# Performance work log

Hardware: AMD Instinct MI355X
Metric: run time of the kernel (lower is better)

Reference implementation:

```python
import jax, jax.numpy as jnp
import numpy as np

TAU = 0.5

def setup_inputs() -> dict:
    key = jax.random.key(0)
    ks = jax.random.split(key, 20)
    B, D1, D2, E1, E2, U = 4096, 2000, 2000, 256, 256, 512
    M = E1 + E2
    s = lambda k, shp, scale=0.05: jax.random.normal(k, shp, dtype=jnp.float32) * scale
    return {
        "inputs": jax.random.normal(ks[0], (B, D1 + D2), dtype=jnp.float32),
        "h_tm1": jax.random.normal(ks[1], (B, U), dtype=jnp.float32),
        "crohis_tm": jax.random.normal(ks[2], (B, M), dtype=jnp.float32),
        "embed_weight_1": s(ks[3], (D1, E1)),
        "embed_weight_2": s(ks[4], (D2, E2)),
        "ca_1to2_w": s(ks[5], (E1, E1)),
        "ca_1to2_u": s(ks[6], (E2, E1)),
        "ca_1to2_v": s(ks[7], (E2, E1)),
        "ca_2to1_w": s(ks[8], (E2, E2)),
        "ca_2to1_u": s(ks[9], (E1, E2)),
        "ca_2to1_v": s(ks[10], (E1, E2)),
        "crohis_weight_w": s(ks[11], (M, U)),
        "crohis_bias": jnp.zeros((U,), jnp.float32),
        "crohis_decomp_weight": s(ks[12], (M, M)),
        "crohis_decomp_bias": jnp.zeros((M,), jnp.float32),
        "kernel": s(ks[13], (M, 3 * U)),
        "recurrent_kernel": s(ks[14], (U, 3 * U)),
        "bias": jnp.zeros((3 * U,), jnp.float32),
    }


def reference(inputs, h_tm1, crohis_tm,
              embed_weight_1, embed_weight_2,
              ca_1to2_w, ca_1to2_u, ca_1to2_v,
              ca_2to1_w, ca_2to1_u, ca_2to1_v,
              crohis_weight_w, crohis_bias,
              crohis_decomp_weight, crohis_decomp_bias,
              kernel, recurrent_kernel, bias):
    D1 = embed_weight_1.shape[0]
    U = recurrent_kernel.shape[0]
    # dual embedding lookups (dense multi-hot x embedding matrix)
    seqx1 = inputs[:, :D1]
    seqx2 = inputs[:, D1:]
    emb1 = seqx1 @ embed_weight_1   # [B, E1]
    emb2 = seqx2 @ embed_weight_2   # [B, E2]
    # cross-attention gates (softmax over feature axis, as K.softmax default)
    att12 = jax.nn.softmax(jnp.tanh(emb1 @ ca_1to2_w + emb2 @ ca_1to2_u) * (emb2 @ ca_1to2_v), axis=-1)
    att21 = jax.nn.softmax(jnp.tanh(emb2 @ ca_2to1_w + emb1 @ ca_2to1_u) * (emb1 @ ca_2to1_v), axis=-1)
    x = jnp.concatenate([emb1 * att12, emb2 * att21], axis=-1)  # [B, M]
    # cross-history decomposition modulating previous hidden state
    cro = jnp.tanh(crohis_tm @ crohis_decomp_weight + crohis_decomp_bias)
    h_prev = h_tm1 + jnp.tanh(cro @ crohis_weight_w + crohis_bias)
    # GRU (implementation=2, reset_after=False)
    mx = x @ kernel + bias                         # [B, 3U]
    x_z, x_r, x_h = mx[:, :U], mx[:, U:2 * U], mx[:, 2 * U:]
    mi = h_prev @ recurrent_kernel[:, :2 * U]      # [B, 2U]
    z = jax.nn.sigmoid(x_z + mi[:, :U])
    r = jax.nn.sigmoid(x_r + mi[:, U:])
    hh = jnp.tanh(x_h + (r * h_prev) @ recurrent_kernel[:, 2 * U:])
    h = z * h_prev + (1.0 - z) * hh
    # updated cross-history state (exponential moving average with tau)
    crohis_new = TAU * crohis_tm + (1.0 - TAU) * x
    return h, crohis_new
```

## Files before the change

### kernel.cpp

```cpp
#include <hip/hip_runtime.h>
#include <hip/hip_bf16.h>
#include <math.h>


#define TAU_F 0.5f

typedef __bf16 bf16x8 __attribute__((ext_vector_type(8)));
typedef __bf16 bf16x4 __attribute__((ext_vector_type(4)));
typedef float f32x4 __attribute__((ext_vector_type(4)));

__device__ __forceinline__ void gload16(const void* g, void* l) {
    __builtin_amdgcn_global_load_lds(
        (const __attribute__((address_space(1))) void*)g,
        (__attribute__((address_space(3))) void*)l, 16, 0, 0);
}

struct SubGemm {
    const void* A;
    int lda;
    int Kvalid;
    const __bf16* BT;
    int ldbt;
    float* C;
    int ldc;
    long long strideC;
    int Ksub;
    int nbx;
    int pairSplit;
    int pairAOff;
};

template <bool AFP32>
__global__ __launch_bounds__(256) void gemm_dual(SubGemm g1, SubGemm g2, int blocks1)
{
    __shared__ __bf16 As[3][64][32];
    __shared__ __bf16 Bs[3][128][32];

    const int tid = threadIdx.x, w = tid >> 6, l = tid & 63;

    const int gx = gridDim.x;
    const int nwg = gx * (int)gridDim.y;
    const int hw = (int)blockIdx.y * gx + (int)blockIdx.x;
    const int lg = (hw & 7) * (nwg >> 3) + (hw >> 3);
    const int bxl_lin = lg % gx;
    const int by = lg / gx;

    const bool second = bxl_lin >= blocks1;
    const SubGemm& g = second ? g2 : g1;
    const int bxl = second ? bxl_lin - blocks1 : bxl_lin;
    const int ct = bxl % g.nbx, spl = bxl / g.nbx;
    const int brow = by * 64, bcol = ct * 128;
    const int k_begin = spl * g.Ksub;
    const int nt = g.Ksub >> 5;
    float* C = g.C + (size_t)spl * g.strideC;
    const int aoff = (ct >= g.pairSplit) ? g.pairAOff : 0;

    const int sar = w * 16 + (l >> 2);
    const int sbr = w * 32 + (l >> 2);
    const int seg = (l & 3) * 8;

    const float*  AfRow = (const float*)g.A + aoff + (size_t)(brow + sar) * g.lda;
    const __bf16* AbRow = (const __bf16*)g.A + aoff + (size_t)(brow + sar) * g.lda + seg + k_begin;
    const __bf16* Bg0 = g.BT + (size_t)(bcol + sbr) * g.ldbt + seg + k_begin;
    const __bf16* Bg1 = Bg0 + (size_t)16 * g.ldbt;
    const int kcl = g.Kvalid - 8;

    f32x4 acc[2][4] = {};
    const int fr = l & 15, fk = (l >> 4) * 8;
    const int wr = (w >> 1) * 32, wc = (w & 1) * 64;

    f32x4 v0, v1;
    if constexpr (AFP32) {
        { int col = k_begin + seg; col = col < kcl ? col : kcl;
          v0 = *(const f32x4*)(AfRow + col); v1 = *(const f32x4*)(AfRow + col + 4); }
        gload16(Bg0, &Bs[0][w * 32][0]);
        gload16(Bg1, &Bs[0][w * 32 + 16][0]);
        asm volatile("s_waitcnt vmcnt(2)" ::: "memory");
        { __bf16 o[8];
#pragma unroll
          for (int z = 0; z < 4; ++z) { o[z] = (__bf16)v0[z]; o[4 + z] = (__bf16)v1[z]; }
          *(bf16x8*)&As[0][sar][seg] = *(bf16x8*)o; }
        { int col = k_begin + 32 + seg; col = col < kcl ? col : kcl;
          v0 = *(const f32x4*)(AfRow + col); v1 = *(const f32x4*)(AfRow + col + 4); }
        gload16(Bg0 + 32, &Bs[1][w * 32][0]);
        gload16(Bg1 + 32, &Bs[1][w * 32 + 16][0]);
    } else {
        gload16(AbRow,      &As[0][w * 16][0]);
        gload16(Bg0,        &Bs[0][w * 32][0]);
        gload16(Bg1,        &Bs[0][w * 32 + 16][0]);
        gload16(AbRow + 32, &As[1][w * 16][0]);
        gload16(Bg0 + 32,   &Bs[1][w * 32][0]);
        gload16(Bg1 + 32,   &Bs[1][w * 32 + 16][0]);
    }

    int b0 = 0, b1 = 1, b2 = 2;
    for (int t = 0; t < nt; ++t) {
        if (t < nt - 1) {
            if constexpr (AFP32) asm volatile("s_waitcnt vmcnt(2)" ::: "memory");
            else                 asm volatile("s_waitcnt vmcnt(3)" ::: "memory");
        } else {
            asm volatile("s_waitcnt vmcnt(0)" ::: "memory");
        }
        asm volatile("s_waitcnt lgkmcnt(0)" ::: "memory");
        __builtin_amdgcn_s_barrier();

        bf16x8 a[2], b[4];
#pragma unroll
        for (int m = 0; m < 2; ++m) a[m] = *(const bf16x8*)&As[b0][wr + m * 16 + fr][fk];
#pragma unroll
        for (int n = 0; n < 4; ++n) b[n] = *(const bf16x8*)&Bs[b0][wc + n * 16 + fr][fk];

        if constexpr (AFP32) {
            if (t + 1 < nt) {
                __bf16 o[8];
#pragma unroll
                for (int z = 0; z < 4; ++z) { o[z] = (__bf16)v0[z]; o[4 + z] = (__bf16)v1[z]; }
                *(bf16x8*)&As[b1][sar][seg] = *(bf16x8*)o;
            }
            if (t + 2 < nt) {
                const int k = (t + 2) * 32;
                int col = k_begin + k + seg; col = col < kcl ? col : kcl;
                v0 = *(const f32x4*)(AfRow + col);
                v1 = *(const f32x4*)(AfRow + col + 4);
                gload16(Bg0 + k, &Bs[b2][w * 32][0]);
                gload16(Bg1 + k, &Bs[b2][w * 32 + 16][0]);
            }
        } else {
            if (t + 2 < nt) {
                const int k = (t + 2) * 32;
                gload16(AbRow + k, &As[b2][w * 16][0]);
                gload16(Bg0 + k,   &Bs[b2][w * 32][0]);
                gload16(Bg1 + k,   &Bs[b2][w * 32 + 16][0]);
            }
        }

#pragma unroll
        for (int m = 0; m < 2; ++m)
#pragma unroll
            for (int n = 0; n < 4; ++n)
                acc[m][n] = __builtin_amdgcn_mfma_f32_16x16x32_bf16(a[m], b[n], acc[m][n], 0, 0, 0);

        const int tmp = b0; b0 = b1; b1 = b2; b2 = tmp;
    }

    const int fq = (l >> 4) * 4;
#pragma unroll
    for (int m = 0; m < 2; ++m)
#pragma unroll
        for (int n = 0; n < 4; ++n)
#pragma unroll
            for (int r = 0; r < 4; ++r) {
                int row = brow + wr + m * 16 + fq + r;
                int col = bcol + wc + n * 16 + fr;
                C[(size_t)row * g.ldc + col] = acc[m][n][r];
            }
}

__global__ __launch_bounds__(256) void prep_w(
    const float* __restrict__ ew1, const float* __restrict__ ew2,
    const float* __restrict__ w12, const float* __restrict__ u12,
    const float* __restrict__ v12, const float* __restrict__ w21,
    const float* __restrict__ u21, const float* __restrict__ v21,
    const float* __restrict__ cd_w, const float* __restrict__ cw_w,
    const float* __restrict__ kern, const float* __restrict__ rkern,
    __bf16* __restrict__ WT, __bf16* __restrict__ WcatT,
    __bf16* __restrict__ cdT, __bf16* __restrict__ cwT,
    __bf16* __restrict__ kernT, __bf16* __restrict__ rkernT)
{
    int idx = blockIdx.x * 256 + threadIdx.x;
    if (idx < 1048576) {
        int n = idx >> 11, k = idx & 2047;
        float v = 0.f;
        if (k < 2000) v = (n < 256) ? ew1[(size_t)k * 256 + n]
                                    : ew2[(size_t)k * 256 + (n - 256)];
        WT[idx] = (__bf16)v;
        return;
    }
    idx -= 1048576;
    if (idx < 524288) {
        int n = idx >> 9, k = idx & 511;
        int jm = n & 255; bool khi = k >= 256; int kk = k & 255;
        float v;
        if (n < 256)      v = khi ? u12[kk * 256 + jm] : w12[kk * 256 + jm];
        else if (n < 512) v = khi ? w21[kk * 256 + jm] : u21[kk * 256 + jm];
        else if (n < 768) v = khi ? v12[kk * 256 + jm] : 0.f;
        else              v = khi ? 0.f : v21[kk * 256 + jm];
        WcatT[idx] = (__bf16)v;
        return;
    }
    idx -= 524288;
    if (idx < 262144) {
        int n = idx >> 9, k = idx & 511;
        cdT[idx] = (__bf16)cd_w[(size_t)k * 512 + n];
        return;
    }
    idx -= 262144;
    if (idx < 262144) {
        int n = idx >> 9, k = idx & 511;
        cwT[idx] = (__bf16)cw_w[(size_t)k * 512 + n];
        return;
    }
    idx -= 262144;
    if (idx < 786432) {
        int n = idx >> 9, k = idx & 511;
        kernT[idx] = (__bf16)kern[(size_t)k * 1536 + n];
        return;
    }
    idx -= 786432;
    if (idx < 786432) {
        int n = idx >> 9, k = idx & 511;
        rkernT[idx] = (__bf16)rkern[(size_t)k * 1536 + n];
    }
}

__global__ __launch_bounds__(256) void reduce_A(
    const float* __restrict__ P12, const float* __restrict__ P4,
    const float* __restrict__ cd_b,
    __bf16* __restrict__ E, __bf16* __restrict__ cro)
{
    int b = blockIdx.x;
    int i = (((b & 2047) * 256) + threadIdx.x) * 4;
    if (b < 2048) {
        f32x4 p0 = *(const f32x4*)(P12 + i);
        f32x4 p1 = *(const f32x4*)(P12 + (1 << 21) + i);
        __bf16 o[4];
#pragma unroll
        for (int j = 0; j < 4; ++j) o[j] = (__bf16)(p0[j] + p1[j]);
        *(bf16x4*)&E[i] = *(bf16x4*)o;
    } else {
        f32x4 p0 = *(const f32x4*)(P4 + i);
        int c = i & 511;
        __bf16 o[4];
#pragma unroll
        for (int j = 0; j < 4; ++j) o[j] = (__bf16)tanhf(p0[j] + cd_b[c + j]);
        *(bf16x4*)&cro[i] = *(bf16x4*)o;
    }
}

__global__ __launch_bounds__(256) void fuse1(
    const float* __restrict__ T, const __bf16* __restrict__ E,
    const float* __restrict__ crohis,
    const float* __restrict__ P5,
    const float* __restrict__ h_tm1, const float* __restrict__ cw_b,
    __bf16* __restrict__ x, float* __restrict__ cro_out,
    float* __restrict__ hprev, __bf16* __restrict__ hprev_bf)
{
    __shared__ float s4[4];
    int b = blockIdx.x;
    int j = threadIdx.x;
    if (b < 4096) {
        const float* t = T + (size_t)b * 1024;
        float s12 = tanhf(t[j])       * t[512 + j];
        float s21 = tanhf(t[256 + j]) * t[768 + j];
        float v = s12;
#pragma unroll
        for (int o = 32; o >= 1; o >>= 1) v = fmaxf(v, __shfl_xor(v, o, 64));
        __syncthreads(); if ((j & 63) == 0) s4[j >> 6] = v; __syncthreads();
        float m12 = fmaxf(fmaxf(s4[0], s4[1]), fmaxf(s4[2], s4[3]));
        float e12 = expf(s12 - m12);
        v = e12;
#pragma unroll
        for (int o = 32; o >= 1; o >>= 1) v += __shfl_xor(v, o, 64);
        __syncthreads(); if ((j & 63) == 0) s4[j >> 6] = v; __syncthreads();
        float sum12 = s4[0] + s4[1] + s4[2] + s4[3];
        v = s21;
#pragma unroll
        for (int o = 32; o >= 1; o >>= 1) v = fmaxf(v, __shfl_xor(v, o, 64));
        __syncthreads(); if ((j & 63) == 0) s4[j >> 6] = v; __syncthreads();
        float m21 = fmaxf(fmaxf(s4[0], s4[1]), fmaxf(s4[2], s4[3]));
        float e21 = expf(s21 - m21);
        v = e21;
#pragma unroll
        for (int o = 32; o >= 1; o >>= 1) v += __shfl_xor(v, o, 64);
        __syncthreads(); if ((j & 63) == 0) s4[j >> 6] = v; __syncthreads();
        float sum21 = s4[0] + s4[1] + s4[2] + s4[3];

        size_t b0 = (size_t)b * 512 + j, b1 = b0 + 256;
        float x1 = (float)E[b0] * (e12 / sum12);
        float x2 = (float)E[b1] * (e21 / sum21);
        x[b0] = (__bf16)x1;
        x[b1] = (__bf16)x2;
        cro_out[b0] = TAU_F * crohis[b0] + (1.f - TAU_F) * x1;
        cro_out[b1] = TAU_F * crohis[b1] + (1.f - TAU_F) * x2;
    } else {
        int i = ((b - 4096) * 256 + j) * 4;
        f32x4 p = *(const f32x4*)(P5 + i);
        f32x4 ht = *(const f32x4*)(h_tm1 + i);
        int c = i & 511;
        f32x4 o; __bf16 ob[4];
#pragma unroll
        for (int q = 0; q < 4; ++q) {
            float hv = ht[q] + tanhf(p[q] + cw_b[c + q]);
            o[q] = hv; ob[q] = (__bf16)hv;
        }
        *(f32x4*)(hprev + i) = o;
        *(bf16x4*)&hprev_bf[i] = *(bf16x4*)ob;
    }
}

__global__ __launch_bounds__(256) void gates_k(
    const float* __restrict__ mx, const float* __restrict__ mi2,
    const float* __restrict__ hprev, const float* __restrict__ bias,
    __bf16* __restrict__ rh)
{
    int i = (blockIdx.x * 256 + threadIdx.x) * 4;
    int row = i >> 9, c = i & 511;
    f32x4 a  = *(const f32x4*)(mx + (size_t)row * 1536 + 512 + c);
    f32x4 m  = *(const f32x4*)(mi2 + (size_t)row * 1024 + 512 + c);
    f32x4 hp = *(const f32x4*)(hprev + i);
    f32x4 bb = *(const f32x4*)(bias + 512 + c);
    __bf16 o[4];
#pragma unroll
    for (int q = 0; q < 4; ++q) {
        float r = 1.f / (1.f + expf(-(a[q] + bb[q] + m[q])));
        o[q] = (__bf16)(r * hp[q]);
    }
    *(bf16x4*)&rh[i] = *(bf16x4*)o;
}

__global__ __launch_bounds__(256) void final_k(
    const float* __restrict__ mx, const float* __restrict__ mi2,
    const float* __restrict__ P8a, const float* __restrict__ P8b,
    const float* __restrict__ hprev, const float* __restrict__ bias,
    float* __restrict__ h)
{
    int i = (blockIdx.x * 256 + threadIdx.x) * 4;
    int row = i >> 9, c = i & 511;
    f32x4 xz = *(const f32x4*)(mx + (size_t)row * 1536 + c);
    f32x4 xh = *(const f32x4*)(mx + (size_t)row * 1536 + 1024 + c);
    f32x4 mz = *(const f32x4*)(mi2 + (size_t)row * 1024 + c);
    f32x4 p0 = *(const f32x4*)(P8a + i);
    f32x4 p1 = *(const f32x4*)(P8b + i);
    f32x4 hp = *(const f32x4*)(hprev + i);
    f32x4 bz = *(const f32x4*)(bias + c);
    f32x4 bh = *(const f32x4*)(bias + 1024 + c);
    f32x4 o;
#pragma unroll
    for (int q = 0; q < 4; ++q) {
        float z = 1.f / (1.f + expf(-(xz[q] + bz[q] + mz[q])));
        float hh = tanhf(xh[q] + bh[q] + p0[q] + p1[q]);
        o[q] = z * hp[q] + (1.f - z) * hh;
    }
    *(f32x4*)(h + i) = o;
}

extern "C" void kernel_launch(void* const* d_in, const int* in_sizes, int n_in,
                              void* d_out, int out_size, void* d_ws, size_t ws_size,
                              hipStream_t stream)
{
    (void)in_sizes; (void)n_in; (void)out_size; (void)ws_size;

    const float* inputs = (const float*)d_in[0];
    const float* h_tm1  = (const float*)d_in[1];
    const float* crohis = (const float*)d_in[2];
    const float* ew1    = (const float*)d_in[3];
    const float* ew2    = (const float*)d_in[4];
    const float* ca12w  = (const float*)d_in[5];
    const float* ca12u  = (const float*)d_in[6];
    const float* ca12v  = (const float*)d_in[7];
    const float* ca21w  = (const float*)d_in[8];
    const float* ca21u  = (const float*)d_in[9];
    const float* ca21v  = (const float*)d_in[10];
    const float* cw_w   = (const float*)d_in[11];
    const float* cw_b   = (const float*)d_in[12];
    const float* cd_w   = (const float*)d_in[13];
    const float* cd_b   = (const float*)d_in[14];
    const float* kern   = (const float*)d_in[15];
    const float* rkern  = (const float*)d_in[16];
    const float* bias   = (const float*)d_in[17];

    char* ws = (char*)d_ws;
    const size_t MB = 1 << 20;
    float*  P12      = (float*)(ws + 0);
    float*  P4       = (float*)(ws + 16 * MB);
    float*  T        = (float*)(ws + 0);
    float*  P5       = (float*)(ws + 16 * MB);
    float*  mx       = (float*)(ws + 0);
    float*  hprev    = (float*)(ws + 24 * MB);
    __bf16* E        = (__bf16*)(ws + 32 * MB);
    __bf16* rh       = (__bf16*)(ws + 32 * MB);
    __bf16* cro_bf   = (__bf16*)(ws + 36 * MB);
    __bf16* x        = (__bf16*)(ws + 36 * MB);
    __bf16* hprev_bf = (__bf16*)(ws + 40 * MB);
    float*  P8       = (float*)(ws + 36 * MB);
    float*  mi2      = (float*)(ws + 44 * MB);
    __bf16* WT       = (__bf16*)(ws + 68 * MB);
    __bf16* WcatT    = (__bf16*)(ws + 70 * MB);
    __bf16* cdT      = (__bf16*)(ws + 71 * MB);
    __bf16* cwT      = (__bf16*)(ws + 71 * MB + 512 * 1024);
    __bf16* kernT    = (__bf16*)(ws + 72 * MB);
    __bf16* rkernT   = (__bf16*)(ws + 73 * MB + 512 * 1024);

    float* h_out   = (float*)d_out;
    float* cro_out = (float*)d_out + 2 * 1048576;

    const int BIG = 1 << 30;

    prep_w<<<14336, 256, 0, stream>>>(ew1, ew2, ca12w, ca12u, ca12v, ca21w,
                                      ca21u, ca21v, cd_w, cw_w, kern, rkern,
                                      WT, WcatT, cdT, cwT, kernT, rkernT);

    SubGemm gA1 = { inputs, 4000, 2000, WT, 2048, P12, 512, 1ll << 21, 1024, 4, 2, 2000 };
    SubGemm gA2 = { crohis,  512,  512, cdT,  512, P4,  512, 0,         512, 4, BIG, 0 };
    gemm_dual<true><<<dim3(12, 64), 256, 0, stream>>>(gA1, gA2, 8);

    reduce_A<<<4096, 256, 0, stream>>>(P12, P4, cd_b, E, cro_bf);

    SubGemm gB1 = { E,      512, 512, WcatT, 512, T,  1024, 0, 512, 8, BIG, 0 };
    SubGemm gB2 = { cro_bf, 512, 512, cwT,   512, P5, 512,  0, 512, 4, BIG, 0 };
    gemm_dual<false><<<dim3(12, 64), 256, 0, stream>>>(gB1, gB2, 8);

    fuse1<<<6144, 256, 0, stream>>>(T, E, crohis, P5, h_tm1, cw_b,
                                    x, cro_out, hprev, hprev_bf);

    SubGemm gC1 = { x,        512, 512, kernT,  512, mx,  1536, 0, 512, 12, BIG, 0 };
    SubGemm gC2 = { hprev_bf, 512, 512, rkernT, 512, mi2, 1024, 0, 512, 8,  BIG, 0 };
    gemm_dual<false><<<dim3(20, 64), 256, 0, stream>>>(gC1, gC2, 12);

    gates_k<<<2048, 256, 0, stream>>>(mx, mi2, hprev, bias, rh);

    SubGemm gG = { rh, 512, 512, rkernT + (size_t)1024 * 512, 512, P8, 512, 6ll << 20, 256, 4, BIG, 0 };
    gemm_dual<false><<<dim3(8, 64), 256, 0, stream>>>(gG, gG, 8);

    final_k<<<2048, 256, 0, stream>>>(mx, mi2, P8, P8 + (6ll << 20), hprev, bias, h_out);
}
```

Measured before the change: 136.9 us.

## Pre-convert activations to bf16 and deepen GEMM pipeline to four LDS stages

The fp32 inputs and crohis are now converted to padded bf16 buffers in the prep kernel, so the first GEMM loads A directly into LDS with global_load_lds instead of doing register loads and conversion inside the main loop. The GEMM drops its fp32 template path and uses a four-buffer ring with a fixed vmcnt wait and clamped prefetch addresses. The weight transposes in the prep kernel now produce eight bf16 values per thread with vector stores. In exchange, the large input matrix takes an extra write and read through the workspace, and the kernel uses more LDS per block.

New measurement: 159.1 us. 16.2% more time.

```diff
diff --git a/kernel.cpp b/kernel.cpp
--- a/kernel.cpp
+++ b/kernel.cpp
@@ -16,9 +16,8 @@
 }
 
 struct SubGemm {
-    const void* A;
+    const __bf16* A;
     int lda;
-    int Kvalid;
     const __bf16* BT;
     int ldbt;
     float* C;
@@ -30,11 +29,10 @@
     int pairAOff;
 };
 
-template <bool AFP32>
 __global__ __launch_bounds__(256) void gemm_dual(SubGemm g1, SubGemm g2, int blocks1)
 {
-    __shared__ __bf16 As[3][64][32];
-    __shared__ __bf16 Bs[3][128][32];
+    __shared__ __bf16 As[4][64][32];
+    __shared__ __bf16 Bs[4][128][32];
 
     const int tid = threadIdx.x, w = tid >> 6, l = tid & 63;
 
@@ -59,89 +57,48 @@
     const int sbr = w * 32 + (l >> 2);
     const int seg = (l & 3) * 8;
 
-    const float*  AfRow = (const float*)g.A + aoff + (size_t)(brow + sar) * g.lda;
-    const __bf16* AbRow = (const __bf16*)g.A + aoff + (size_t)(brow + sar) * g.lda + seg + k_begin;
+    const __bf16* Ar  = g.A + aoff + (size_t)(brow + sar) * g.lda + seg + k_begin;
     const __bf16* Bg0 = g.BT + (size_t)(bcol + sbr) * g.ldbt + seg + k_begin;
     const __bf16* Bg1 = Bg0 + (size_t)16 * g.ldbt;
-    const int kcl = g.Kvalid - 8;
 
     f32x4 acc[2][4] = {};
     const int fr = l & 15, fk = (l >> 4) * 8;
     const int wr = (w >> 1) * 32, wc = (w & 1) * 64;
-
-    f32x4 v0, v1;
-    if constexpr (AFP32) {
-        { int col = k_begin + seg; col = col < kcl ? col : kcl;
-          v0 = *(const f32x4*)(AfRow + col); v1 = *(const f32x4*)(AfRow + col + 4); }
-        gload16(Bg0, &Bs[0][w * 32][0]);
-        gload16(Bg1, &Bs[0][w * 32 + 16][0]);
-        asm volatile("s_waitcnt vmcnt(2)" ::: "memory");
-        { __bf16 o[8];
-#pragma unroll
-          for (int z = 0; z < 4; ++z) { o[z] = (__bf16)v0[z]; o[4 + z] = (__bf16)v1[z]; }
-          *(bf16x8*)&As[0][sar][seg] = *(bf16x8*)o; }
-        { int col = k_begin + 32 + seg; col = col < kcl ? col : kcl;
-          v0 = *(const f32x4*)(AfRow + col); v1 = *(const f32x4*)(AfRow + col + 4); }
-        gload16(Bg0 + 32, &Bs[1][w * 32][0]);
-        gload16(Bg1 + 32, &Bs[1][w * 32 + 16][0]);
-    } else {
-        gload16(AbRow,      &As[0][w * 16][0]);
-        gload16(Bg0,        &Bs[0][w * 32][0]);
-        gload16(Bg1,        &Bs[0][w * 32 + 16][0]);
-        gload16(AbRow + 32, &As[1][w * 16][0]);
-        gload16(Bg0 + 32,   &Bs[1][w * 32][0]);
-        gload16(Bg1 + 32,   &Bs[1][w * 32 + 16][0]);
-    }
-
-    int b0 = 0, b1 = 1, b2 = 2;
+    const int kmax = (nt - 1) * 32;
+
+#define ISSUE(slot)                                                        \
+    {                                                                      \
+        const int _s = (slot);                                             \
+        const int _k = (_s * 32 < kmax) ? _s * 32 : kmax;                  \
+        const int _b = _s & 3;                                             \
+        gload16(Ar + _k,  &As[_b][w * 16][0]);                             \
+        gload16(Bg0 + _k, &Bs[_b][w * 32][0]);                             \
+        gload16(Bg1 + _k, &Bs[_b][w * 32 + 16][0]);                        \
+    }
+
+    ISSUE(0) ISSUE(1) ISSUE(2)
+
     for (int t = 0; t < nt; ++t) {
-        if (t < nt - 1) {
-            if constexpr (AFP32) asm volatile("s_waitcnt vmcnt(2)" ::: "memory");
-            else                 asm volatile("s_waitcnt vmcnt(3)" ::: "memory");
-        } else {
-            asm volatile("s_waitcnt vmcnt(0)" ::: "memory");
-        }
+        asm volatile("s_waitcnt vmcnt(6)" ::: "memory");
         asm volatile("s_waitcnt lgkmcnt(0)" ::: "memory");
         __builtin_amdgcn_s_barrier();
 
+        const int bi = t & 3;
         bf16x8 a[2], b[4];
 #pragma unroll
-        for (int m = 0; m < 2; ++m) a[m] = *(const bf16x8*)&As[b0][wr + m * 16 + fr][fk];
-#pragma unroll
-        for (int n = 0; n < 4; ++n) b[n] = *(const bf16x8*)&Bs[b0][wc + n * 16 + fr][fk];
-
-        if constexpr (AFP32) {
-            if (t + 1 < nt) {
-                __bf16 o[8];
-#pragma unroll
-                for (int z = 0; z < 4; ++z) { o[z] = (__bf16)v0[z]; o[4 + z] = (__bf16)v1[z]; }
-                *(bf16x8*)&As[b1][sar][seg] = *(bf16x8*)o;
-            }
-            if (t + 2 < nt) {
-                const int k = (t + 2) * 32;
-                int col = k_begin + k + seg; col = col < kcl ? col : kcl;
-                v0 = *(const f32x4*)(AfRow + col);
-                v1 = *(const f32x4*)(AfRow + col + 4);
-                gload16(Bg0 + k, &Bs[b2][w * 32][0]);
-                gload16(Bg1 + k, &Bs[b2][w * 32 + 16][0]);
-            }
-        } else {
-            if (t + 2 < nt) {
-                const int k = (t + 2) * 32;
-                gload16(AbRow + k, &As[b2][w * 16][0]);
-                gload16(Bg0 + k,   &Bs[b2][w * 32][0]);
-                gload16(Bg1 + k,   &Bs[b2][w * 32 + 16][0]);
-            }
-        }
+        for (int m = 0; m < 2; ++m) a[m] = *(const bf16x8*)&As[bi][wr + m * 16 + fr][fk];
+#pragma unroll
+        for (int n = 0; n < 4; ++n) b[n] = *(const bf16x8*)&Bs[bi][wc + n * 16 + fr][fk];
+
+        ISSUE(t + 3)
 
 #pragma unroll
         for (int m = 0; m < 2; ++m)
 #pragma unroll
             for (int n = 0; n < 4; ++n)
                 acc[m][n] = __builtin_amdgcn_mfma_f32_16x16x32_bf16(a[m], b[n], acc[m][n], 0, 0, 0);
-
-        const int tmp = b0; b0 = b1; b1 = b2; b2 = tmp;
-    }
+    }
+#undef ISSUE
 
     const int fq = (l >> 4) * 4;
 #pragma unroll
@@ -156,60 +113,127 @@
             }
 }
 
-__global__ __launch_bounds__(256) void prep_w(
+__global__ __launch_bounds__(256) void prep_all(
+    const float* __restrict__ inputs, const float* __restrict__ crohis,
     const float* __restrict__ ew1, const float* __restrict__ ew2,
     const float* __restrict__ w12, const float* __restrict__ u12,
     const float* __restrict__ v12, const float* __restrict__ w21,
     const float* __restrict__ u21, const float* __restrict__ v21,
     const float* __restrict__ cd_w, const float* __restrict__ cw_w,
     const float* __restrict__ kern, const float* __restrict__ rkern,
+    __bf16* __restrict__ Xb, __bf16* __restrict__ crohis_bf,
     __bf16* __restrict__ WT, __bf16* __restrict__ WcatT,
     __bf16* __restrict__ cdT, __bf16* __restrict__ cwT,
     __bf16* __restrict__ kernT, __bf16* __restrict__ rkernT)
 {
-    int idx = blockIdx.x * 256 + threadIdx.x;
-    if (idx < 1048576) {
-        int n = idx >> 11, k = idx & 2047;
-        float v = 0.f;
-        if (k < 2000) v = (n < 256) ? ew1[(size_t)k * 256 + n]
-                                    : ew2[(size_t)k * 256 + (n - 256)];
-        WT[idx] = (__bf16)v;
-        return;
-    }
-    idx -= 1048576;
-    if (idx < 524288) {
-        int n = idx >> 9, k = idx & 511;
-        int jm = n & 255; bool khi = k >= 256; int kk = k & 255;
-        float v;
-        if (n < 256)      v = khi ? u12[kk * 256 + jm] : w12[kk * 256 + jm];
-        else if (n < 512) v = khi ? w21[kk * 256 + jm] : u21[kk * 256 + jm];
-        else if (n < 768) v = khi ? v12[kk * 256 + jm] : 0.f;
-        else              v = khi ? 0.f : v21[kk * 256 + jm];
-        WcatT[idx] = (__bf16)v;
-        return;
-    }
-    idx -= 524288;
-    if (idx < 262144) {
-        int n = idx >> 9, k = idx & 511;
-        cdT[idx] = (__bf16)cd_w[(size_t)k * 512 + n];
-        return;
-    }
-    idx -= 262144;
-    if (idx < 262144) {
-        int n = idx >> 9, k = idx & 511;
-        cwT[idx] = (__bf16)cw_w[(size_t)k * 512 + n];
-        return;
-    }
-    idx -= 262144;
-    if (idx < 786432) {
-        int n = idx >> 9, k = idx & 511;
-        kernT[idx] = (__bf16)kern[(size_t)k * 1536 + n];
-        return;
-    }
-    idx -= 786432;
-    if (idx < 786432) {
-        int n = idx >> 9, k = idx & 511;
-        rkernT[idx] = (__bf16)rkern[(size_t)k * 1536 + n];
+    int i = blockIdx.x * 256 + threadIdx.x;
+    if (i < 1024000) {
+        int r = i / 250, c = (i - r * 250) * 8;
+        const float* p = inputs + (size_t)r * 4000 + c;
+        f32x4 v0 = *(const f32x4*)p, v1 = *(const f32x4*)(p + 4);
+        __bf16 o[8];
+#pragma unroll
+        for (int z = 0; z < 4; ++z) { o[z] = (__bf16)v0[z]; o[4 + z] = (__bf16)v1[z]; }
+        *(bf16x8*)(Xb + (size_t)r * 4096 + c) = *(bf16x8*)o;
+        return;
+    }
+    i -= 1024000;
+    if (i < 1024000) {
+        int r = i / 250, c = (i - r * 250) * 8;
+        const float* p = inputs + (size_t)r * 4000 + 2000 + c;
+        f32x4 v0 = *(const f32x4*)p, v1 = *(const f32x4*)(p + 4);
+        __bf16 o[8];
+#pragma unroll
+        for (int z = 0; z < 4; ++z) { o[z] = (__bf16)v0[z]; o[4 + z] = (__bf16)v1[z]; }
+        *(bf16x8*)(Xb + (size_t)r * 4096 + 2048 + c) = *(bf16x8*)o;
+        return;
+    }
+    i -= 1024000;
+    if (i < 49152) {
+        int r = i / 12, gg = i - r * 12;
+        int c = (gg < 6) ? 2000 + gg * 8 : 4048 + (gg - 6) * 8;
+        __bf16 o[8] = {};
+        *(bf16x8*)(Xb + (size_t)r * 4096 + c) = *(bf16x8*)o;
+        return;
+    }
+    i -= 49152;
+    if (i < 262144) {
+        int e = i * 8;
+        const float* p = crohis + e;
+        f32x4 v0 = *(const f32x4*)p, v1 = *(const f32x4*)(p + 4);
+        __bf16 o[8];
+#pragma unroll
+        for (int z = 0; z < 4; ++z) { o[z] = (__bf16)v0[z]; o[4 + z] = (__bf16)v1[z]; }
+        *(bf16x8*)(crohis_bf + e) = *(bf16x8*)o;
+        return;
+    }
+    i -= 262144;
+    if (i < 131072) {
+        int e = i * 8, n = e >> 11, k0 = e & 2047;
+        __bf16 o[8];
+#pragma unroll
+        for (int z = 0; z < 8; ++z) {
+            int k = k0 + z;
+            float v = 0.f;
+            if (k < 2000) v = (n < 256) ? ew1[(size_t)k * 256 + n]
+                                        : ew2[(size_t)k * 256 + (n - 256)];
+            o[z] = (__bf16)v;
+        }
+        *(bf16x8*)(WT + e) = *(bf16x8*)o;
+        return;
+    }
+    i -= 131072;
+    if (i < 65536) {
+        int e = i * 8, n = e >> 9, k0 = e & 511;
+        int jm = n & 255;
+        __bf16 o[8];
+#pragma unroll
+        for (int z = 0; z < 8; ++z) {
+            int k = k0 + z; bool khi = k >= 256; int kk = k & 255;
+            float v;
+            if (n < 256)      v = khi ? u12[kk * 256 + jm] : w12[kk * 256 + jm];
+            else if (n < 512) v = khi ? w21[kk * 256 + jm] : u21[kk * 256 + jm];
+            else if (n < 768) v = khi ? v12[kk * 256 + jm] : 0.f;
+            else              v = khi ? 0.f : v21[kk * 256 + jm];
+            o[z] = (__bf16)v;
+        }
+        *(bf16x8*)(WcatT + e) = *(bf16x8*)o;
+        return;
+    }
+    i -= 65536;
+    if (i < 32768) {
+        int e = i * 8, n = e >> 9, k0 = e & 511;
+        __bf16 o[8];
+#pragma unroll
+        for (int z = 0; z < 8; ++z) o[z] = (__bf16)cd_w[(size_t)(k0 + z) * 512 + n];
+        *(bf16x8*)(cdT + e) = *(bf16x8*)o;
+        return;
+    }
+    i -= 32768;
+    if (i < 32768) {
+        int e = i * 8, n = e >> 9, k0 = e & 511;
+        __bf16 o[8];
+#pragma unroll
+        for (int z = 0; z < 8; ++z) o[z] = (__bf16)cw_w[(size_t)(k0 + z) * 512 + n];
+        *(bf16x8*)(cwT + e) = *(bf16x8*)o;
+        return;
+    }
+    i -= 32768;
+    if (i < 98304) {
+        int e = i * 8, n = e >> 9, k0 = e & 511;
+        __bf16 o[8];
+#pragma unroll
+        for (int z = 0; z < 8; ++z) o[z] = (__bf16)kern[(size_t)(k0 + z) * 1536 + n];
+        *(bf16x8*)(kernT + e) = *(bf16x8*)o;
+        return;
+    }
+    i -= 98304;
+    if (i < 98304) {
+        int e = i * 8, n = e >> 9, k0 = e & 511;
+        __bf16 o[8];
+#pragma unroll
+        for (int z = 0; z < 8; ++z) o[z] = (__bf16)rkern[(size_t)(k0 + z) * 1536 + n];
+        *(bf16x8*)(rkernT + e) = *(bf16x8*)o;
     }
 }
 
@@ -371,56 +395,61 @@
 
     char* ws = (char*)d_ws;
     const size_t MB = 1 << 20;
-    float*  P12      = (float*)(ws + 0);
-    float*  P4       = (float*)(ws + 16 * MB);
-    float*  T        = (float*)(ws + 0);
-    float*  P5       = (float*)(ws + 16 * MB);
-    float*  mx       = (float*)(ws + 0);
-    float*  hprev    = (float*)(ws + 24 * MB);
-    __bf16* E        = (__bf16*)(ws + 32 * MB);
-    __bf16* rh       = (__bf16*)(ws + 32 * MB);
-    __bf16* cro_bf   = (__bf16*)(ws + 36 * MB);
-    __bf16* x        = (__bf16*)(ws + 36 * MB);
-    __bf16* hprev_bf = (__bf16*)(ws + 40 * MB);
-    float*  P8       = (float*)(ws + 36 * MB);
-    float*  mi2      = (float*)(ws + 44 * MB);
-    __bf16* WT       = (__bf16*)(ws + 68 * MB);
-    __bf16* WcatT    = (__bf16*)(ws + 70 * MB);
-    __bf16* cdT      = (__bf16*)(ws + 71 * MB);
-    __bf16* cwT      = (__bf16*)(ws + 71 * MB + 512 * 1024);
-    __bf16* kernT    = (__bf16*)(ws + 72 * MB);
-    __bf16* rkernT   = (__bf16*)(ws + 73 * MB + 512 * 1024);
+    float*  P12       = (float*)(ws + 0);
+    float*  P4        = (float*)(ws + 16 * MB);
+    __bf16* Xb        = (__bf16*)(ws + 24 * MB);
+    __bf16* crohis_bf = (__bf16*)(ws + 56 * MB);
+    __bf16* E         = (__bf16*)(ws + 32 * MB);
+    __bf16* cro_bf    = (__bf16*)(ws + 36 * MB);
+    float*  T         = (float*)(ws + 0);
+    float*  P5        = (float*)(ws + 16 * MB);
+    __bf16* x         = (__bf16*)(ws + 40 * MB);
+    float*  hprev     = (float*)(ws + 24 * MB);
+    __bf16* hprev_bf  = (__bf16*)(ws + 64 * MB);
+    float*  mx        = (float*)(ws + 0);
+    float*  mi2       = (float*)(ws + 44 * MB);
+    __bf16* rh        = (__bf16*)(ws + 32 * MB);
+    float*  P8        = (float*)(ws + 36 * MB);
+    float*  P8b       = (float*)(ws + 60 * MB);
+    __bf16* WT        = (__bf16*)(ws + 68 * MB);
+    __bf16* WcatT     = (__bf16*)(ws + 70 * MB);
+    __bf16* cdT       = (__bf16*)(ws + 71 * MB);
+    __bf16* cwT       = (__bf16*)(ws + 71 * MB + 512 * 1024);
+    __bf16* kernT     = (__bf16*)(ws + 72 * MB);
+    __bf16* rkernT    = (__bf16*)(ws + 73 * MB + 512 * 1024);
 
     float* h_out   = (float*)d_out;
     float* cro_out = (float*)d_out + 2 * 1048576;
 
     const int BIG = 1 << 30;
 
-    prep_w<<<14336, 256, 0, stream>>>(ew1, ew2, ca12w, ca12u, ca12v, ca21w,
-                                      ca21u, ca21v, cd_w, cw_w, kern, rkern,
-                                      WT, WcatT, cdT, cwT, kernT, rkernT);
-
-    SubGemm gA1 = { inputs, 4000, 2000, WT, 2048, P12, 512, 1ll << 21, 1024, 4, 2, 2000 };
-    SubGemm gA2 = { crohis,  512,  512, cdT,  512, P4,  512, 0,         512, 4, BIG, 0 };
-    gemm_dual<true><<<dim3(12, 64), 256, 0, stream>>>(gA1, gA2, 8);
+    prep_all<<<11008, 256, 0, stream>>>(inputs, crohis, ew1, ew2,
+                                        ca12w, ca12u, ca12v, ca21w, ca21u, ca21v,
+                                        cd_w, cw_w, kern, rkern,
+                                        Xb, crohis_bf, WT, WcatT, cdT, cwT,
+                                        kernT, rkernT);
+
+    SubGemm gA1 = { Xb,        4096, WT,  2048, P12, 512, 1ll << 21, 1024, 4, 2, 2048 };
+    SubGemm gA2 = { crohis_bf,  512, cdT,  512, P4,  512, 0,          512, 4, BIG, 0 };
+    gemm_dual<<<dim3(12, 64), 256, 0, stream>>>(gA1, gA2, 8);
 
     reduce_A<<<4096, 256, 0, stream>>>(P12, P4, cd_b, E, cro_bf);
 
-    SubGemm gB1 = { E,      512, 512, WcatT, 512, T,  1024, 0, 512, 8, BIG, 0 };
-    SubGemm gB2 = { cro_bf, 512, 512, cwT,   512, P5, 512,  0, 512, 4, BIG, 0 };
-    gemm_dual<false><<<dim3(12, 64), 256, 0, stream>>>(gB1, gB2, 8);
+    SubGemm gB1 = { E,      512, WcatT, 512, T,  1024, 0, 512, 8, BIG, 0 };
+    SubGemm gB2 = { cro_bf, 512, cwT,   512, P5, 512,  0, 512, 4, BIG, 0 };
+    gemm_dual<<<dim3(12, 64), 256, 0, stream>>>(gB1, gB2, 8);
 
     fuse1<<<6144, 256, 0, stream>>>(T, E, crohis, P5, h_tm1, cw_b,
                                     x, cro_out, hprev, hprev_bf);
 
-    SubGemm gC1 = { x,        512, 512, kernT,  512, mx,  1536, 0, 512, 12, BIG, 0 };
-    SubGemm gC2 = { hprev_bf, 512, 512, rkernT, 512, mi2, 1024, 0, 512, 8,  BIG, 0 };
-    gemm_dual<false><<<dim3(20, 64), 256, 0, stream>>>(gC1, gC2, 12);
+    SubGemm gC1 = { x,        512, kernT,  512, mx,  1536, 0, 512, 12, BIG, 0 };
+    SubGemm gC2 = { hprev_bf, 512, rkernT, 512, mi2, 1024, 0, 512, 8,  BIG, 0 };
+    gemm_dual<<<dim3(20, 64), 256, 0, stream>>>(gC1, gC2, 12);
 
     gates_k<<<2048, 256, 0, stream>>>(mx, mi2, hprev, bias, rh);
 
-    SubGemm gG = { rh, 512, 512, rkernT + (size_t)1024 * 512, 512, P8, 512, 6ll << 20, 256, 4, BIG, 0 };
-    gemm_dual<false><<<dim3(8, 64), 256, 0, stream>>>(gG, gG, 8);
-
-    final_k<<<2048, 256, 0, stream>>>(mx, mi2, P8, P8 + (6ll << 20), hprev, bias, h_out);
-}
+    SubGemm gG = { rh, 512, rkernT + (size_t)1024 * 512, 512, P8, 512, 6ll << 20, 256, 4, BIG, 0 };
+    gemm_dual<<<dim3(8, 64), 256, 0, stream>>>(gG, gG, 8);
+
+    final_k<<<2048, 256, 0, stream>>>(mx, mi2, P8, P8b, hprev, bias, h_out);
+}
```

## Deepen GEMM prefetch to four LDS stages and tile-transpose weight prep

Applied to the files above, without the earlier changes.

The GEMM main loop moves from a 3-buffer to a 4-buffer LDS ring. Loads are issued three tiles ahead, with addresses clamped so the loop needs no tail branches. The fp32-A path keeps several register stages in flight and is unrolled by four. The weight preparation kernel is rewritten as a 64x64 shared-memory tile transpose, so global reads and writes are coalesced instead of strided, and workspace offsets are rearranged. Risks are extra LDS per block, which can lower occupancy, and the unroll-by-four loop assumes the tile count is a multiple of four.

After: 134.5 us. Within noise of the previous version (-1.8%).

```diff
diff --git a/kernel.cpp b/kernel.cpp
--- a/kernel.cpp
+++ b/kernel.cpp
@@ -33,8 +33,8 @@
 template <bool AFP32>
 __global__ __launch_bounds__(256) void gemm_dual(SubGemm g1, SubGemm g2, int blocks1)
 {
-    __shared__ __bf16 As[3][64][32];
-    __shared__ __bf16 Bs[3][128][32];
+    __shared__ __bf16 As[4][64][32];
+    __shared__ __bf16 Bs[4][128][32];
 
     const int tid = threadIdx.x, w = tid >> 6, l = tid & 63;
 
@@ -59,8 +59,8 @@
     const int sbr = w * 32 + (l >> 2);
     const int seg = (l & 3) * 8;
 
-    const float*  AfRow = (const float*)g.A + aoff + (size_t)(brow + sar) * g.lda;
-    const __bf16* AbRow = (const __bf16*)g.A + aoff + (size_t)(brow + sar) * g.lda + seg + k_begin;
+    const __bf16* Ab  = (const __bf16*)g.A + aoff + (size_t)(brow + sar) * g.lda + seg + k_begin;
+    const float*  Af  = (const float*)g.A + aoff + (size_t)(brow + sar) * g.lda;
     const __bf16* Bg0 = g.BT + (size_t)(bcol + sbr) * g.ldbt + seg + k_begin;
     const __bf16* Bg1 = Bg0 + (size_t)16 * g.ldbt;
     const int kcl = g.Kvalid - 8;
@@ -68,80 +68,97 @@
     f32x4 acc[2][4] = {};
     const int fr = l & 15, fk = (l >> 4) * 8;
     const int wr = (w >> 1) * 32, wc = (w & 1) * 64;
-
-    f32x4 v0, v1;
+    const int kmax = (nt - 1) * 32;
+
+#define ISSUE_B(slot)                                                      \
+    {                                                                      \
+        const int _s = (slot);                                             \
+        const int _k = (_s * 32 < kmax) ? _s * 32 : kmax;                  \
+        const int _b = _s & 3;                                             \
+        gload16(Bg0 + _k, &Bs[_b][w * 32][0]);                             \
+        gload16(Bg1 + _k, &Bs[_b][w * 32 + 16][0]);                        \
+    }
+#define ISSUE_AB(slot)                                                     \
+    {                                                                      \
+        const int _s = (slot);                                             \
+        const int _k = (_s * 32 < kmax) ? _s * 32 : kmax;                  \
+        const int _b = _s & 3;                                             \
+        gload16(Ab + _k,  &As[_b][w * 16][0]);                             \
+        gload16(Bg0 + _k, &Bs[_b][w * 32][0]);                             \
+        gload16(Bg1 + _k, &Bs[_b][w * 32 + 16][0]);                        \
+    }
+
     if constexpr (AFP32) {
-        { int col = k_begin + seg; col = col < kcl ? col : kcl;
-          v0 = *(const f32x4*)(AfRow + col); v1 = *(const f32x4*)(AfRow + col + 4); }
-        gload16(Bg0, &Bs[0][w * 32][0]);
-        gload16(Bg1, &Bs[0][w * 32 + 16][0]);
-        asm volatile("s_waitcnt vmcnt(2)" ::: "memory");
-        { __bf16 o[8];
-#pragma unroll
-          for (int z = 0; z < 4; ++z) { o[z] = (__bf16)v0[z]; o[4 + z] = (__bf16)v1[z]; }
-          *(bf16x8*)&As[0][sar][seg] = *(bf16x8*)o; }
-        { int col = k_begin + 32 + seg; col = col < kcl ? col : kcl;
-          v0 = *(const f32x4*)(AfRow + col); v1 = *(const f32x4*)(AfRow + col + 4); }
-        gload16(Bg0 + 32, &Bs[1][w * 32][0]);
-        gload16(Bg1 + 32, &Bs[1][w * 32 + 16][0]);
+        f32x4 r0a, r0b, r1a, r1b, r2a, r2b, r3a, r3b;
+
+        auto aload = [&](int slot, f32x4& ra, f32x4& rb) {
+            int c = k_begin + slot * 32 + seg;
+            c = c < kcl ? c : kcl;
+            ra = *(const f32x4*)(Af + c);
+            rb = *(const f32x4*)(Af + c + 4);
+        };
+        auto awrite = [&](int bufi, f32x4& ra, f32x4& rb) {
+            __bf16 o[8];
+#pragma unroll
+            for (int z = 0; z < 4; ++z) { o[z] = (__bf16)ra[z]; o[4 + z] = (__bf16)rb[z]; }
+            *(bf16x8*)&As[bufi][sar][seg] = *(bf16x8*)o;
+        };
+        auto astep = [&](int t, f32x4& wa, f32x4& wb, f32x4& la, f32x4& lb) {
+            asm volatile("s_waitcnt vmcnt(4)" ::: "memory");
+            asm volatile("s_waitcnt lgkmcnt(0)" ::: "memory");
+            __builtin_amdgcn_s_barrier();
+            const int bi = t & 3;
+            bf16x8 a[2], b[4];
+#pragma unroll
+            for (int m = 0; m < 2; ++m) a[m] = *(const bf16x8*)&As[bi][wr + m * 16 + fr][fk];
+#pragma unroll
+            for (int n = 0; n < 4; ++n) b[n] = *(const bf16x8*)&Bs[bi][wc + n * 16 + fr][fk];
+            awrite((t + 1) & 3, wa, wb);
+            aload(t + 3, la, lb);
+            ISSUE_B(t + 2)
+#pragma unroll
+            for (int m = 0; m < 2; ++m)
+#pragma unroll
+                for (int n = 0; n < 4; ++n)
+                    acc[m][n] = __builtin_amdgcn_mfma_f32_16x16x32_bf16(a[m], b[n], acc[m][n], 0, 0, 0);
+        };
+
+        aload(0, r0a, r0b);
+        asm volatile("s_waitcnt vmcnt(0)" ::: "memory");
+        awrite(0, r0a, r0b);
+        aload(1, r1a, r1b);
+        ISSUE_B(0)
+        aload(2, r2a, r2b);
+        ISSUE_B(1)
+
+        for (int t = 0; t < nt; t += 4) {
+            astep(t,     r1a, r1b, r3a, r3b);
+            astep(t + 1, r2a, r2b, r0a, r0b);
+            astep(t + 2, r3a, r3b, r1a, r1b);
+            astep(t + 3, r0a, r0b, r2a, r2b);
+        }
     } else {
-        gload16(AbRow,      &As[0][w * 16][0]);
-        gload16(Bg0,        &Bs[0][w * 32][0]);
-        gload16(Bg1,        &Bs[0][w * 32 + 16][0]);
-        gload16(AbRow + 32, &As[1][w * 16][0]);
-        gload16(Bg0 + 32,   &Bs[1][w * 32][0]);
-        gload16(Bg1 + 32,   &Bs[1][w * 32 + 16][0]);
-    }
-
-    int b0 = 0, b1 = 1, b2 = 2;
-    for (int t = 0; t < nt; ++t) {
-        if (t < nt - 1) {
-            if constexpr (AFP32) asm volatile("s_waitcnt vmcnt(2)" ::: "memory");
-            else                 asm volatile("s_waitcnt vmcnt(3)" ::: "memory");
-        } else {
-            asm volatile("s_waitcnt vmcnt(0)" ::: "memory");
+        ISSUE_AB(0) ISSUE_AB(1) ISSUE_AB(2)
+        for (int t = 0; t < nt; ++t) {
+            asm volatile("s_waitcnt vmcnt(6)" ::: "memory");
+            asm volatile("s_waitcnt lgkmcnt(0)" ::: "memory");
+            __builtin_amdgcn_s_barrier();
+            const int bi = t & 3;
+            bf16x8 a[2], b[4];
+#pragma unroll
+            for (int m = 0; m < 2; ++m) a[m] = *(const bf16x8*)&As[bi][wr + m * 16 + fr][fk];
+#pragma unroll
+            for (int n = 0; n < 4; ++n) b[n] = *(const bf16x8*)&Bs[bi][wc + n * 16 + fr][fk];
+            ISSUE_AB(t + 3)
+#pragma unroll
+            for (int m = 0; m < 2; ++m)
+#pragma unroll
+                for (int n = 0; n < 4; ++n)
+                    acc[m][n] = __builtin_amdgcn_mfma_f32_16x16x32_bf16(a[m], b[n], acc[m][n], 0, 0, 0);
         }
-        asm volatile("s_waitcnt lgkmcnt(0)" ::: "memory");
-        __builtin_amdgcn_s_barrier();
-
-        bf16x8 a[2], b[4];
-#pragma unroll
-        for (int m = 0; m < 2; ++m) a[m] = *(const bf16x8*)&As[b0][wr + m * 16 + fr][fk];
-#pragma unroll
-        for (int n = 0; n < 4; ++n) b[n] = *(const bf16x8*)&Bs[b0][wc + n * 16 + fr][fk];
-
-        if constexpr (AFP32) {
-            if (t + 1 < nt) {
-                __bf16 o[8];
-#pragma unroll
-                for (int z = 0; z < 4; ++z) { o[z] = (__bf16)v0[z]; o[4 + z] = (__bf16)v1[z]; }
-                *(bf16x8*)&As[b1][sar][seg] = *(bf16x8*)o;
-            }
-            if (t + 2 < nt) {
-                const int k = (t + 2) * 32;
-                int col = k_begin + k + seg; col = col < kcl ? col : kcl;
-                v0 = *(const f32x4*)(AfRow + col);
-                v1 = *(const f32x4*)(AfRow + col + 4);
-                gload16(Bg0 + k, &Bs[b2][w * 32][0]);
-                gload16(Bg1 + k, &Bs[b2][w * 32 + 16][0]);
-            }
-        } else {
-            if (t + 2 < nt) {
-                const int k = (t + 2) * 32;
-                gload16(AbRow + k, &As[b2][w * 16][0]);
-                gload16(Bg0 + k,   &Bs[b2][w * 32][0]);
-                gload16(Bg1 + k,   &Bs[b2][w * 32 + 16][0]);
-            }
-        }
-
-#pragma unroll
-        for (int m = 0; m < 2; ++m)
-#pragma unroll
-            for (int n = 0; n < 4; ++n)
-                acc[m][n] = __builtin_amdgcn_mfma_f32_16x16x32_bf16(a[m], b[n], acc[m][n], 0, 0, 0);
-
-        const int tmp = b0; b0 = b1; b1 = b2; b2 = tmp;
-    }
+    }
+#undef ISSUE_B
+#undef ISSUE_AB
 
     const int fq = (l >> 4) * 4;
 #pragma unroll
@@ -156,7 +173,7 @@
             }
 }
 
-__global__ __launch_bounds__(256) void prep_w(
+__global__ __launch_bounds__(256) void prep_wT(
     const float* __restrict__ ew1, const float* __restrict__ ew2,
     const float* __restrict__ w12, const float* __restrict__ u12,
     const float* __restrict__ v12, const float* __restrict__ w21,
@@ -167,49 +184,54 @@
     __bf16* __restrict__ cdT, __bf16* __restrict__ cwT,
     __bf16* __restrict__ kernT, __bf16* __restrict__ rkernT)
 {
-    int idx = blockIdx.x * 256 + threadIdx.x;
-    if (idx < 1048576) {
-        int n = idx >> 11, k = idx & 2047;
+    __shared__ float tile[64][65];
+    const int b = blockIdx.x, tid = threadIdx.x;
+    const int tr = tid >> 6, tc = tid & 63;
+
+    const float* src = nullptr;
+    int ldsrc = 0, srow0 = 0, scol0 = 0, kvalid = 1 << 30;
+    __bf16* dst; int ldd, n0, k0;
+    bool zero = false;
+
+    if (b < 256) {
+        int q = b; n0 = (q >> 5) * 64; k0 = (q & 31) * 64;
+        dst = WT; ldd = 2048; kvalid = 2000; ldsrc = 256; srow0 = k0;
+        if (n0 < 256) { src = ew1; scol0 = n0; } else { src = ew2; scol0 = n0 - 256; }
+    } else if (b < 384) {
+        int q = b - 256; n0 = (q >> 3) * 64; k0 = (q & 7) * 64;
+        dst = WcatT; ldd = 512; ldsrc = 256; srow0 = k0 & 255; scol0 = n0 & 255;
+        int qn = n0 >> 8; bool khi = k0 >= 256;
+        if (qn == 0)      src = khi ? u12 : w12;
+        else if (qn == 1) src = khi ? w21 : u21;
+        else if (qn == 2) { if (khi) src = v12; else zero = true; }
+        else              { if (khi) zero = true; else src = v21; }
+    } else if (b < 448) {
+        int q = b - 384; n0 = (q >> 3) * 64; k0 = (q & 7) * 64;
+        src = cd_w; ldsrc = 512; srow0 = k0; scol0 = n0; dst = cdT; ldd = 512;
+    } else if (b < 512) {
+        int q = b - 448; n0 = (q >> 3) * 64; k0 = (q & 7) * 64;
+        src = cw_w; ldsrc = 512; srow0 = k0; scol0 = n0; dst = cwT; ldd = 512;
+    } else if (b < 704) {
+        int q = b - 512; n0 = (q >> 3) * 64; k0 = (q & 7) * 64;
+        src = kern; ldsrc = 1536; srow0 = k0; scol0 = n0; dst = kernT; ldd = 512;
+    } else {
+        int q = b - 704; n0 = (q >> 3) * 64; k0 = (q & 7) * 64;
+        src = rkern; ldsrc = 1536; srow0 = k0; scol0 = n0; dst = rkernT; ldd = 512;
+    }
+
+#pragma unroll
+    for (int p = 0; p < 16; ++p) {
+        int kr = p * 4 + tr;
         float v = 0.f;
-        if (k < 2000) v = (n < 256) ? ew1[(size_t)k * 256 + n]
-                                    : ew2[(size_t)k * 256 + (n - 256)];
-        WT[idx] = (__bf16)v;
-        return;
-    }
-    idx -= 1048576;
-    if (idx < 524288) {
-        int n = idx >> 9, k = idx & 511;
-        int jm = n & 255; bool khi = k >= 256; int kk = k & 255;
-        float v;
-        if (n < 256)      v = khi ? u12[kk * 256 + jm] : w12[kk * 256 + jm];
-        else if (n < 512) v = khi ? w21[kk * 256 + jm] : u21[kk * 256 + jm];
-        else if (n < 768) v = khi ? v12[kk * 256 + jm] : 0.f;
-        else              v = khi ? 0.f : v21[kk * 256 + jm];
-        WcatT[idx] = (__bf16)v;
-        return;
-    }
-    idx -= 524288;
-    if (idx < 262144) {
-        int n = idx >> 9, k = idx & 511;
-        cdT[idx] = (__bf16)cd_w[(size_t)k * 512 + n];
-        return;
-    }
-    idx -= 262144;
-    if (idx < 262144) {
-        int n = idx >> 9, k = idx & 511;
-        cwT[idx] = (__bf16)cw_w[(size_t)k * 512 + n];
-        return;
-    }
-    idx -= 262144;
-    if (idx < 786432) {
-        int n = idx >> 9, k = idx & 511;
-        kernT[idx] = (__bf16)kern[(size_t)k * 1536 + n];
-        return;
-    }
-    idx -= 786432;
-    if (idx < 786432) {
-        int n = idx >> 9, k = idx & 511;
-        rkernT[idx] = (__bf16)rkern[(size_t)k * 1536 + n];
+        if (!zero && (srow0 + kr) < kvalid)
+            v = src[(size_t)(srow0 + kr) * ldsrc + scol0 + tc];
+        tile[kr][tc] = v;
+    }
+    __syncthreads();
+#pragma unroll
+    for (int p = 0; p < 16; ++p) {
+        int nr = p * 4 + tr;
+        dst[(size_t)(n0 + nr) * ldd + k0 + tc] = (__bf16)tile[tc][nr];
     }
 }
 
@@ -373,17 +395,18 @@
     const size_t MB = 1 << 20;
     float*  P12      = (float*)(ws + 0);
     float*  P4       = (float*)(ws + 16 * MB);
+    __bf16* E        = (__bf16*)(ws + 32 * MB);
+    __bf16* cro_bf   = (__bf16*)(ws + 36 * MB);
     float*  T        = (float*)(ws + 0);
     float*  P5       = (float*)(ws + 16 * MB);
+    __bf16* x        = (__bf16*)(ws + 40 * MB);
+    float*  hprev    = (float*)(ws + 24 * MB);
+    __bf16* hprev_bf = (__bf16*)(ws + 64 * MB);
     float*  mx       = (float*)(ws + 0);
-    float*  hprev    = (float*)(ws + 24 * MB);
-    __bf16* E        = (__bf16*)(ws + 32 * MB);
+    float*  mi2      = (float*)(ws + 44 * MB);
     __bf16* rh       = (__bf16*)(ws + 32 * MB);
-    __bf16* cro_bf   = (__bf16*)(ws + 36 * MB);
-    __bf16* x        = (__bf16*)(ws + 36 * MB);
-    __bf16* hprev_bf = (__bf16*)(ws + 40 * MB);
     float*  P8       = (float*)(ws + 36 * MB);
-    float*  mi2      = (float*)(ws + 44 * MB);
+    float*  P8b      = (float*)(ws + 60 * MB);
     __bf16* WT       = (__bf16*)(ws + 68 * MB);
     __bf16* WcatT    = (__bf16*)(ws + 70 * MB);
     __bf16* cdT      = (__bf16*)(ws + 71 * MB);
@@ -396,12 +419,12 @@
 
     const int BIG = 1 << 30;
 
-    prep_w<<<14336, 256, 0, stream>>>(ew1, ew2, ca12w, ca12u, ca12v, ca21w,
-                                      ca21u, ca21v, cd_w, cw_w, kern, rkern,
-                                      WT, WcatT, cdT, cwT, kernT, rkernT);
-
-    SubGemm gA1 = { inputs, 4000, 2000, WT, 2048, P12, 512, 1ll << 21, 1024, 4, 2, 2000 };
-    SubGemm gA2 = { crohis,  512,  512, cdT,  512, P4,  512, 0,         512, 4, BIG, 0 };
+    prep_wT<<<896, 256, 0, stream>>>(ew1, ew2, ca12w, ca12u, ca12v, ca21w,
+                                     ca21u, ca21v, cd_w, cw_w, kern, rkern,
+                                     WT, WcatT, cdT, cwT, kernT, rkernT);
+
+    SubGemm gA1 = { inputs, 4000, 2000, WT,  2048, P12, 512, 1ll << 21, 1024, 4, 2, 2000 };
+    SubGemm gA2 = { crohis,  512,  512, cdT,  512, P4,  512, 0,          512, 4, BIG, 0 };
     gemm_dual<true><<<dim3(12, 64), 256, 0, stream>>>(gA1, gA2, 8);
 
     reduce_A<<<4096, 256, 0, stream>>>(P12, P4, cd_b, E, cro_bf);
@@ -422,5 +445,5 @@
     SubGemm gG = { rh, 512, 512, rkernT + (size_t)1024 * 512, 512, P8, 512, 6ll << 20, 256, 4, BIG, 0 };
     gemm_dual<false><<<dim3(8, 64), 256, 0, stream>>>(gG, gG, 8);
 
-    final_k<<<2048, 256, 0, stream>>>(mx, mi2, P8, P8 + (6ll << 20), hprev, bias, h_out);
-}
+    final_k<<<2048, 256, 0, stream>>>(mx, mi2, P8, P8b, hprev, bias, h_out);
+}
```
